# Performance work log

Measured on AMD Instinct MI355X. Metric: run time of the kernel, lower is better.

The kernel has to match this reference:

```python
import jax, jax.numpy as jnp
import numpy as np


def setup_inputs() -> dict:
    key = jax.random.key(0)
    k1, k2, k3 = jax.random.split(key, 3)
    b, h, w = 16, 512, 512
    affinity = jax.random.normal(k1, (b, 9, h, w), dtype=jnp.float32)
    cur_seg = jax.random.normal(k2, (b, 1, h, w), dtype=jnp.float32)
    coarse_seg = jax.random.normal(k3, (b, 1, h, w), dtype=jnp.float32)
    return {"affinity": affinity, "cur_seg": cur_seg, "coarse_seg": coarse_seg, "i": 0}


def _unfold3x3(x):
    # x: [b, 1, h, w] -> patches [b, 9, h, w], ordering matches nn.Unfold
    # (row-major over (ky, kx)), patch k at (i,j) = x[i+ky-1, j+kx-1] (zero pad)
    b, _, h, w = x.shape
    xp = jnp.pad(x[:, 0], ((0, 0), (1, 1), (1, 1)))  # [b, h+2, w+2]
    patches = [xp[:, dy:dy + h, dx:dx + w] for dy in range(3) for dx in range(3)]
    return jnp.stack(patches, axis=1)  # [b, 9, h, w]


def reference(affinity, cur_seg, coarse_seg, i):
    b, c, h, w = affinity.shape  # c == 9
    patches = _unfold3x3(cur_seg)                      # [b, 9, h, w]
    # replace center tap with coarse_seg (as in cur_seg_unfold[:, 4] = ...)
    patches = patches.at[:, 4].set(coarse_seg[:, 0])
    out = jnp.sum(patches * affinity, axis=1, keepdims=True)  # [b, 1, h, w]
    return out
```

## Files before the change

kernel.cpp:

```cpp
#include <hip/hip_runtime.h>


__global__ __launch_bounds__(256) void cspn_kernel(
    const float* __restrict__ aff,
    const float* __restrict__ cur,
    const float* __restrict__ coarse,
    float* __restrict__ out,
    int B, int H, int W)
{
    const int W4 = W >> 2;
    const int total = B * H * W4;
    int t = blockIdx.x * blockDim.x + threadIdx.x;
    if (t >= total) return;

    const int xq   = t % W4;
    const int rest = t / W4;
    const int y    = rest % H;
    const int b    = rest / H;
    const int x0   = xq << 2;

    const size_t plane = (size_t)H * W;
    const float* curb  = cur + (size_t)b * plane;
    const size_t rowoff = (size_t)y * W + x0;

    float4 md = *(const float4*)(curb + rowoff);
    float mdl = 0.f, mdr = 0.f;
    if (x0 > 0)     mdl = curb[rowoff - 1];
    if (x0 + 4 < W) mdr = curb[rowoff + 4];

    float4 up = make_float4(0.f, 0.f, 0.f, 0.f);
    float upl = 0.f, upr = 0.f;
    if (y > 0) {
        const size_t o = rowoff - (size_t)W;
        up = *(const float4*)(curb + o);
        if (x0 > 0)     upl = curb[o - 1];
        if (x0 + 4 < W) upr = curb[o + 4];
    }

    float4 dn = make_float4(0.f, 0.f, 0.f, 0.f);
    float dnl = 0.f, dnr = 0.f;
    if (y + 1 < H) {
        const size_t o = rowoff + (size_t)W;
        dn = *(const float4*)(curb + o);
        if (x0 > 0)     dnl = curb[o - 1];
        if (x0 + 4 < W) dnr = curb[o + 4];
    }

    float4 co = *(const float4*)(coarse + (size_t)b * plane + rowoff);

    const float* affb = aff + (size_t)b * 9 * plane + rowoff;
    float4 a[9];
    #pragma unroll
    for (int k = 0; k < 9; ++k)
        a[k] = *(const float4*)(affb + (size_t)k * plane);

    float4 r;
    r.x = a[0].x*upl  + a[1].x*up.x + a[2].x*up.y
        + a[3].x*mdl  + a[4].x*co.x + a[5].x*md.y
        + a[6].x*dnl  + a[7].x*dn.x + a[8].x*dn.y;
    r.y = a[0].y*up.x + a[1].y*up.y + a[2].y*up.z
        + a[3].y*md.x + a[4].y*co.y + a[5].y*md.z
        + a[6].y*dn.x + a[7].y*dn.y + a[8].y*dn.z;
    r.z = a[0].z*up.y + a[1].z*up.z + a[2].z*up.w
        + a[3].z*md.y + a[4].z*co.z + a[5].z*md.w
        + a[6].z*dn.y + a[7].z*dn.z + a[8].z*dn.w;
    r.w = a[0].w*up.z + a[1].w*up.w + a[2].w*upr
        + a[3].w*md.z + a[4].w*co.w + a[5].w*mdr
        + a[6].w*dn.z + a[7].w*dn.w + a[8].w*dnr;

    *(float4*)(out + (size_t)b * plane + rowoff) = r;
}

extern "C" void kernel_launch(void* const* d_in, const int* in_sizes, int n_in,
                              void* d_out, int out_size, void* d_ws, size_t ws_size,
                              hipStream_t stream) {
    const float* aff    = (const float*)d_in[0];
    const float* cur    = (const float*)d_in[1];
    const float* coarse = (const float*)d_in[2];
    float* out = (float*)d_out;

    const int B = 16, H = 512, W = 512;
    const int total = B * H * (W >> 2);
    const int block = 256;
    const int grid  = (total + block - 1) / block;

    cspn_kernel<<<grid, block, 0, stream>>>(aff, cur, coarse, out, B, H, W);
}
```

Before: 237.5 us.

## Map one wavefront per row with lane shuffles for halos and nontemporal accesses

Each 64-lane wavefront now processes a full 512-wide row, eight pixels per lane, and gets left/right neighbour values from adjacent lanes via shuffles instead of extra scalar loads. Affinity reads and output writes use nontemporal builtins, and problem sizes become compile-time constants, which removes division and modulo indexing. The aim is fewer, wider memory transactions and less cache pollution from streamed data. It hardcodes the shape and relies on rows matching the wavefront width.

```diff
diff --git a/kernel.cpp b/kernel.cpp
--- a/kernel.cpp
+++ b/kernel.cpp
@@ -1,74 +1,81 @@
 #include <hip/hip_runtime.h>
 
+
+typedef float f4 __attribute__((ext_vector_type(4)));
+
+constexpr int Bc = 16, Hc = 512, Wc = 512;
 
 __global__ __launch_bounds__(256) void cspn_kernel(
     const float* __restrict__ aff,
     const float* __restrict__ cur,
     const float* __restrict__ coarse,
-    float* __restrict__ out,
-    int B, int H, int W)
+    float* __restrict__ out)
 {
-    const int W4 = W >> 2;
-    const int total = B * H * W4;
-    int t = blockIdx.x * blockDim.x + threadIdx.x;
-    if (t >= total) return;
+    const int lane = threadIdx.x & 63;
+    const int row  = (blockIdx.x << 2) + (threadIdx.x >> 6);
+    const int y    = row & (Hc - 1);
+    const int b    = row >> 9;
+    const int plane = Hc * Wc;
+    const int rb   = row * Wc;
+    const int xo   = lane << 3;
 
-    const int xq   = t % W4;
-    const int rest = t / W4;
-    const int y    = rest % H;
-    const int b    = rest / H;
-    const int x0   = xq << 2;
+    const float* curp = cur + rb + xo;
 
-    const size_t plane = (size_t)H * W;
-    const float* curb  = cur + (size_t)b * plane;
-    const size_t rowoff = (size_t)y * W + x0;
+    f4 mp = *(const f4*)(curp);
+    f4 mq = *(const f4*)(curp + 4);
+    f4 up = (f4)(0.f), uq = (f4)(0.f), dp = (f4)(0.f), dq = (f4)(0.f);
+    if (y > 0)      { up = *(const f4*)(curp - Wc); uq = *(const f4*)(curp - Wc + 4); }
+    if (y < Hc - 1) { dp = *(const f4*)(curp + Wc); dq = *(const f4*)(curp + Wc + 4); }
+    f4 cp = *(const f4*)(coarse + rb + xo);
+    f4 cq = *(const f4*)(coarse + rb + xo + 4);
 
-    float4 md = *(const float4*)(curb + rowoff);
-    float mdl = 0.f, mdr = 0.f;
-    if (x0 > 0)     mdl = curb[rowoff - 1];
-    if (x0 + 4 < W) mdr = curb[rowoff + 4];
+    float uL = __shfl_up(uq.w, 1);   if (lane == 0)  uL = 0.f;
+    float mL = __shfl_up(mq.w, 1);   if (lane == 0)  mL = 0.f;
+    float dL = __shfl_up(dq.w, 1);   if (lane == 0)  dL = 0.f;
+    float uR = __shfl_down(up.x, 1); if (lane == 63) uR = 0.f;
+    float mR = __shfl_down(mp.x, 1); if (lane == 63) mR = 0.f;
+    float dR = __shfl_down(dp.x, 1); if (lane == 63) dR = 0.f;
 
-    float4 up = make_float4(0.f, 0.f, 0.f, 0.f);
-    float upl = 0.f, upr = 0.f;
-    if (y > 0) {
-        const size_t o = rowoff - (size_t)W;
-        up = *(const float4*)(curb + o);
-        if (x0 > 0)     upl = curb[o - 1];
-        if (x0 + 4 < W) upr = curb[o + 4];
-    }
+    const float u[10] = {uL, up.x,up.y,up.z,up.w, uq.x,uq.y,uq.z,uq.w, uR};
+    const float m[10] = {mL, mp.x,mp.y,mp.z,mp.w, mq.x,mq.y,mq.z,mq.w, mR};
+    const float d[10] = {dL, dp.x,dp.y,dp.z,dp.w, dq.x,dq.y,dq.z,dq.w, dR};
+    const float c[8]  = {cp.x,cp.y,cp.z,cp.w, cq.x,cq.y,cq.z,cq.w};
 
-    float4 dn = make_float4(0.f, 0.f, 0.f, 0.f);
-    float dnl = 0.f, dnr = 0.f;
-    if (y + 1 < H) {
-        const size_t o = rowoff + (size_t)W;
-        dn = *(const float4*)(curb + o);
-        if (x0 > 0)     dnl = curb[o - 1];
-        if (x0 + 4 < W) dnr = curb[o + 4];
-    }
+    const float* ab = aff + b * 9 * plane + y * Wc + xo;
 
-    float4 co = *(const float4*)(coarse + (size_t)b * plane + rowoff);
+    float acc[8];
 
-    const float* affb = aff + (size_t)b * 9 * plane + rowoff;
-    float4 a[9];
-    #pragma unroll
-    for (int k = 0; k < 9; ++k)
-        a[k] = *(const float4*)(affb + (size_t)k * plane);
+#define TAP0(K, S) {                                                          \
+    f4 A0 = __builtin_nontemporal_load((const f4*)(ab + (K) * plane));        \
+    f4 A1 = __builtin_nontemporal_load((const f4*)(ab + (K) * plane + 4));    \
+    acc[0] = A0.x*(S)[0]; acc[1] = A0.y*(S)[1];                               \
+    acc[2] = A0.z*(S)[2]; acc[3] = A0.w*(S)[3];                               \
+    acc[4] = A1.x*(S)[4]; acc[5] = A1.y*(S)[5];                               \
+    acc[6] = A1.z*(S)[6]; acc[7] = A1.w*(S)[7]; }
+#define TAP(K, S) {                                                           \
+    f4 A0 = __builtin_nontemporal_load((const f4*)(ab + (K) * plane));        \
+    f4 A1 = __builtin_nontemporal_load((const f4*)(ab + (K) * plane + 4));    \
+    acc[0] += A0.x*(S)[0]; acc[1] += A0.y*(S)[1];                             \
+    acc[2] += A0.z*(S)[2]; acc[3] += A0.w*(S)[3];                             \
+    acc[4] += A1.x*(S)[4]; acc[5] += A1.y*(S)[5];                             \
+    acc[6] += A1.z*(S)[6]; acc[7] += A1.w*(S)[7]; }
 
-    float4 r;
-    r.x = a[0].x*upl  + a[1].x*up.x + a[2].x*up.y
-        + a[3].x*mdl  + a[4].x*co.x + a[5].x*md.y
-        + a[6].x*dnl  + a[7].x*dn.x + a[8].x*dn.y;
-    r.y = a[0].y*up.x + a[1].y*up.y + a[2].y*up.z
-        + a[3].y*md.x + a[4].y*co.y + a[5].y*md.z
-        + a[6].y*dn.x + a[7].y*dn.y + a[8].y*dn.z;
-    r.z = a[0].z*up.y + a[1].z*up.z + a[2].z*up.w
-        + a[3].z*md.y + a[4].z*co.z + a[5].z*md.w
-        + a[6].z*dn.y + a[7].z*dn.z + a[8].z*dn.w;
-    r.w = a[0].w*up.z + a[1].w*up.w + a[2].w*upr
-        + a[3].w*md.z + a[4].w*co.w + a[5].w*mdr
-        + a[6].w*dn.z + a[7].w*dn.w + a[8].w*dnr;
+    TAP0(0, u);
+    TAP (1, u + 1);
+    TAP (2, u + 2);
+    TAP (3, m);
+    TAP (4, c);
+    TAP (5, m + 2);
+    TAP (6, d);
+    TAP (7, d + 1);
+    TAP (8, d + 2);
+#undef TAP0
+#undef TAP
 
-    *(float4*)(out + (size_t)b * plane + rowoff) = r;
+    f4 r0 = {acc[0], acc[1], acc[2], acc[3]};
+    f4 r1 = {acc[4], acc[5], acc[6], acc[7]};
+    __builtin_nontemporal_store(r0, (f4*)(out + rb + xo));
+    __builtin_nontemporal_store(r1, (f4*)(out + rb + xo + 4));
 }
 
 extern "C" void kernel_launch(void* const* d_in, const int* in_sizes, int n_in,
@@ -79,10 +86,9 @@
     const float* coarse = (const float*)d_in[2];
     float* out = (float*)d_out;
 
-    const int B = 16, H = 512, W = 512;
-    const int total = B * H * (W >> 2);
+    const int rows  = Bc * Hc;
     const int block = 256;
-    const int grid  = (total + block - 1) / block;
+    const int grid  = rows / 4;
 
-    cspn_kernel<<<grid, block, 0, stream>>>(aff, cur, coarse, out, B, H, W);
+    cspn_kernel<<<grid, block, 0, stream>>>(aff, cur, coarse, out);
 }
```

Result: no change. 236.9 us (-0.2%).
